# Kernel tuning notes

Measured on AMD Instinct MI355X. Metric: run time of the kernel, lower is better.

Reference implementation:

```python
import jax, jax.numpy as jnp
import numpy as np

B, T, D, U = 2, 512, 768, 768


def setup_inputs() -> dict:
    key = jax.random.key(0)
    kx, kv, ku, kw = jax.random.split(key, 4)
    x = jax.random.normal(kx, (B, T, D), dtype=jnp.float32)
    # glorot-ish scaled params
    V_a = jax.random.normal(kv, (U,), dtype=jnp.float32) * (1.0 / np.sqrt(U))
    U_a = jax.random.normal(ku, (D, U), dtype=jnp.float32) * (1.0 / np.sqrt(D))
    b_u = jnp.zeros((U,), dtype=jnp.float32)
    W_a = jax.random.normal(kw, (D, U), dtype=jnp.float32) * (1.0 / np.sqrt(D))
    return {"x": x, "V_a": V_a, "U_a": U_a, "b_u": b_u, "W_a": W_a}


def reference(x, V_a, U_a, b_u, W_a):
    # Bahdanau additive self-attention, fully batched (replaces the per-timestep loop).
    # wx[b,i,u] = x[b,i] @ W_a  (query projection; original recomputed this per step)
    wx = jnp.einsum('bid,du->biu', x, W_a)
    # ux[b,j,u] = x[b,j] @ U_a + b_u  (the _uxpb term)
    ux = jnp.einsum('bjd,du->bju', x, U_a) + b_u
    # e[b,i,j] = V_a . tanh(wx[b,i] + ux[b,j])
    e = jnp.einsum('biju,u->bij', jnp.tanh(wx[:, :, None, :] + ux[:, None, :, :]), V_a)
    # original: exp / sum over keys == softmax over axis j (no mask path)
    at = jax.nn.softmax(e, axis=2)
    # context[b,i,d] = sum_j at[b,i,j] * x[b,j,d]
    return jnp.einsum('bij,bjd->bid', at, x)
```

## Files before the change

kernel.cpp:

```cpp
#include <hip/hip_runtime.h>
#include <hip/hip_bf16.h>

#define BB 2
#define TT 512
#define DD 768
#define UU 768
#define NR (BB*TT)
#define CC 2.8853900817779268f

typedef __attribute__((ext_vector_type(8))) short short8v;
typedef __attribute__((ext_vector_type(4))) float float4v;
typedef __attribute__((ext_vector_type(4))) unsigned short ushort4v;

static __device__ __forceinline__ float fexp2(float x) { return __builtin_amdgcn_exp2f(x); }
static __device__ __forceinline__ float frcp(float x)  { return __builtin_amdgcn_rcpf(x); }
static __device__ __forceinline__ float readlane_f(float v, int l) {
    return __builtin_bit_cast(float, __builtin_amdgcn_readlane(__builtin_bit_cast(unsigned, v), l));
}
static __device__ __forceinline__ unsigned short bf16rn(float f) {
    unsigned u = __builtin_bit_cast(unsigned, f);
    u += 0x7FFFu + ((u >> 16) & 1u);
    return (unsigned short)(u >> 16);
}
static __device__ __forceinline__ float bf16tof(unsigned short h) {
    return __builtin_bit_cast(float, ((unsigned)h) << 16);
}

__global__ __launch_bounds__(256) void prep_split(
    const float* __restrict__ x,
    const float* __restrict__ Wm,
    const float* __restrict__ Um,
    unsigned short* __restrict__ xhi, unsigned short* __restrict__ xlo,
    unsigned short* __restrict__ WThi, unsigned short* __restrict__ WTlo,
    unsigned short* __restrict__ UThi, unsigned short* __restrict__ UTlo)
{
    const int mode = blockIdx.z;
    const int t = threadIdx.x;

    if (mode == 2) {
        const int blk = blockIdx.y * 12 + blockIdx.x;
        const float4* src = (const float4*)x + (size_t)blk * 1024;
        #pragma unroll
        for (int i = 0; i < 4; ++i) {
            const int idx = i * 256 + t;
            const float4 v = src[idx];
            ushort4v h, l;
            h.x = bf16rn(v.x); l.x = bf16rn(v.x - bf16tof(h.x));
            h.y = bf16rn(v.y); l.y = bf16rn(v.y - bf16tof(h.y));
            h.z = bf16rn(v.z); l.z = bf16rn(v.z - bf16tof(h.z));
            h.w = bf16rn(v.w); l.w = bf16rn(v.w - bf16tof(h.w));
            const size_t off = (size_t)blk * 4096 + (size_t)idx * 4;
            *(ushort4v*)(xhi + off) = h;
            *(ushort4v*)(xlo + off) = l;
        }
        return;
    }
    if (blockIdx.y >= 12) return;

    const float* __restrict__ S = (mode == 0) ? Wm : Um;
    unsigned short* __restrict__ Thi = (mode == 0) ? WThi : UThi;
    unsigned short* __restrict__ Tlo = (mode == 0) ? WTlo : UTlo;

    __shared__ float tile[64][65];
    const int d0 = blockIdx.y * 64;
    const int u0 = blockIdx.x * 64;

    #pragma unroll
    for (int i = 0; i < 4; ++i) {
        const int f4 = i * 256 + t;
        const int r  = f4 >> 4;
        const int c4 = f4 & 15;
        const float4 v = *(const float4*)(S + (size_t)(d0 + r) * UU + u0 + c4 * 4);
        tile[r][c4 * 4 + 0] = v.x;
        tile[r][c4 * 4 + 1] = v.y;
        tile[r][c4 * 4 + 2] = v.z;
        tile[r][c4 * 4 + 3] = v.w;
    }
    __syncthreads();
    #pragma unroll
    for (int i = 0; i < 2; ++i) {
        const int cid = i * 256 + t;
        const int ur  = cid >> 3;
        const int kc  = cid & 7;
        short8v H, L;
        #pragma unroll
        for (int j = 0; j < 8; ++j) {
            const float f = tile[kc * 8 + j][ur];
            const unsigned short h = bf16rn(f);
            H[j] = (short)h;
            L[j] = (short)bf16rn(f - bf16tof(h));
        }
        const size_t off = (size_t)(u0 + ur) * DD + d0 + kc * 8;
        *(short8v*)(Thi + off) = H;
        *(short8v*)(Tlo + off) = L;
    }
}

__global__ __launch_bounds__(256) void gemm_mfma(
    const unsigned short* __restrict__ xhi, const unsigned short* __restrict__ xlo,
    const unsigned short* __restrict__ WThi, const unsigned short* __restrict__ WTlo,
    const unsigned short* __restrict__ UThi, const unsigned short* __restrict__ UTlo,
    const float* __restrict__ bu,
    float* __restrict__ EW4,
    float* __restrict__ EUT)
{
    const int mode = blockIdx.z;
    const unsigned short* __restrict__ Ahi = mode ? UThi : WThi;
    const unsigned short* __restrict__ Alo = mode ? UTlo : WTlo;

    __shared__ unsigned short lds[4 * 4096];

    const int tid  = threadIdx.x;
    const int lane = tid & 63;
    const int wid  = tid >> 6;
    const int wm   = wid >> 1, wn = wid & 1;
    const int u0   = blockIdx.y * 64;
    const int r0t  = blockIdx.x * 64;

    const int srow0 = tid >> 3;
    const int srow1 = srow0 + 32;
    const int sc0   = tid & 7;
    const int sw0   = (sc0 ^ (srow0 & 7)) << 3;

    short8v g0, g1, g2, g3, g4, g5, g6, g7;

#define LOADSTEP(K0) { \
    const size_t ka = (size_t)(K0) + sc0 * 8; \
    g0 = *(const short8v*)(Ahi + (size_t)(u0 + srow0) * DD + ka); \
    g1 = *(const short8v*)(Ahi + (size_t)(u0 + srow1) * DD + ka); \
    g2 = *(const short8v*)(Alo + (size_t)(u0 + srow0) * DD + ka); \
    g3 = *(const short8v*)(Alo + (size_t)(u0 + srow1) * DD + ka); \
    g4 = *(const short8v*)(xhi + (size_t)(r0t + srow0) * DD + ka); \
    g5 = *(const short8v*)(xhi + (size_t)(r0t + srow1) * DD + ka); \
    g6 = *(const short8v*)(xlo + (size_t)(r0t + srow0) * DD + ka); \
    g7 = *(const short8v*)(xlo + (size_t)(r0t + srow1) * DD + ka); }

#define WRITESTEP { \
    *(short8v*)&lds[0 * 4096 + srow0 * 64 + sw0] = g0; \
    *(short8v*)&lds[0 * 4096 + srow1 * 64 + sw0] = g1; \
    *(short8v*)&lds[1 * 4096 + srow0 * 64 + sw0] = g2; \
    *(short8v*)&lds[1 * 4096 + srow1 * 64 + sw0] = g3; \
    *(short8v*)&lds[2 * 4096 + srow0 * 64 + sw0] = g4; \
    *(short8v*)&lds[2 * 4096 + srow1 * 64 + sw0] = g5; \
    *(short8v*)&lds[3 * 4096 + srow0 * 64 + sw0] = g6; \
    *(short8v*)&lds[3 * 4096 + srow1 * 64 + sw0] = g7; }

    float4v acc[2][2] = {};

    LOADSTEP(0);
    for (int s = 0; s < 12; ++s) {
        __syncthreads();
        WRITESTEP;
        __syncthreads();
        if (s < 11) LOADSTEP((s + 1) * 64);

        short8v ah[2][2], al[2][2], bh[2][2], bl[2][2];
        #pragma unroll
        for (int f = 0; f < 2; ++f) {
            const int arow = wm * 32 + f * 16 + (lane & 15);
            const int brow = wn * 32 + f * 16 + (lane & 15);
            #pragma unroll
            for (int kk = 0; kk < 2; ++kk) {
                const int ck = kk * 4 + (lane >> 4);
                ah[f][kk] = *(const short8v*)&lds[0 * 4096 + arow * 64 + (((ck ^ (arow & 7))) << 3)];
                al[f][kk] = *(const short8v*)&lds[1 * 4096 + arow * 64 + (((ck ^ (arow & 7))) << 3)];
                bh[f][kk] = *(const short8v*)&lds[2 * 4096 + brow * 64 + (((ck ^ (brow & 7))) << 3)];
                bl[f][kk] = *(const short8v*)&lds[3 * 4096 + brow * 64 + (((ck ^ (brow & 7))) << 3)];
            }
        }
        #pragma unroll
        for (int kk = 0; kk < 2; ++kk)
            #pragma unroll
            for (int m = 0; m < 2; ++m)
                #pragma unroll
                for (int n = 0; n < 2; ++n) {
                    acc[m][n] = __builtin_amdgcn_mfma_f32_16x16x32_bf16(ah[m][kk], bh[n][kk], acc[m][n], 0, 0, 0);
                    acc[m][n] = __builtin_amdgcn_mfma_f32_16x16x32_bf16(ah[m][kk], bl[n][kk], acc[m][n], 0, 0, 0);
                    acc[m][n] = __builtin_amdgcn_mfma_f32_16x16x32_bf16(al[m][kk], bh[n][kk], acc[m][n], 0, 0, 0);
                }
    }

    #pragma unroll
    for (int m = 0; m < 2; ++m) {
        #pragma unroll
        for (int n = 0; n < 2; ++n) {
            const int ub = u0 + wm * 32 + m * 16 + ((lane >> 4) << 2);
            const int r  = r0t + wn * 32 + n * 16 + (lane & 15);
            if (mode == 0) {
                float* dst = EW4 + ((size_t)(r >> 2) * UU + ub) * 4 + (r & 3);
                #pragma unroll
                for (int reg = 0; reg < 4; ++reg)
                    dst[reg * 4] = fexp2(acc[m][n][reg] * CC);
            } else {
                const int b = r >> 9, j = r & 511;
                const float4 bv = *(const float4*)(bu + ub);
                float4v o;
                o[0] = fexp2((acc[m][n][0] + bv.x) * CC);
                o[1] = fexp2((acc[m][n][1] + bv.y) * CC);
                o[2] = fexp2((acc[m][n][2] + bv.z) * CC);
                o[3] = fexp2((acc[m][n][3] + bv.w) * CC);
                *(float4v*)(EUT + (size_t)b * (UU * TT) + (size_t)(ub >> 2) * (TT * 4) + j * 4) = o;
            }
        }
    }
#undef LOADSTEP
#undef WRITESTEP
}

__global__ __launch_bounds__(512) void attn_fused(
    const float* __restrict__ x,
    const float* __restrict__ V_a,
    const float* __restrict__ EW4,
    const float* __restrict__ EUT,
    float* __restrict__ out)
{
    extern __shared__ float smem[];
    float* part = smem;
    float* red  = smem;

    const int tid  = threadIdx.x;
    const int lane = tid & 63;
    const int w    = tid >> 6;

    const int bid = blockIdx.x;
    const int blk = (bid & 7) * 32 + (bid >> 3);

    const int r0 = blk * 4;
    const int b  = r0 >> 9;

    const float4* __restrict__ ew4q = (const float4*)EW4 + (size_t)blk * UU;
    const float4* __restrict__ vp4  = (const float4*)V_a;
    const float4* __restrict__ eq   = (const float4*)(EUT + (size_t)b * UU * TT) + tid;

    float acc0 = 0.f, acc1 = 0.f, acc2 = 0.f, acc3 = 0.f;

#define ROW4(E4, S0, S1, S2, S3, V4, F, ACC) { \
    const float d0 = fmaf((E4).x, S0.F, 1.f); \
    const float d1 = fmaf((E4).y, S1.F, 1.f); \
    const float d2 = fmaf((E4).z, S2.F, 1.f); \
    const float d3 = fmaf((E4).w, S3.F, 1.f); \
    float n01 = (V4).x * d1; n01 = fmaf((V4).y, d0, n01); \
    float n23 = (V4).z * d3; n23 = fmaf((V4).w, d2, n23); \
    const float dd01 = d0 * d1, dd23 = d2 * d3; \
    float n = n01 * dd23; n = fmaf(n23, dd01, n); \
    ACC = fmaf(n, frcp(dd01 * dd23), ACC); }
#define QUAD4(E4, q) { \
    const float4 S0 = ew4q[4 * (q)]; \
    const float4 S1 = ew4q[4 * (q) + 1]; \
    const float4 S2 = ew4q[4 * (q) + 2]; \
    const float4 S3 = ew4q[4 * (q) + 3]; \
    const float4 V4 = vp4[(q)]; \
    ROW4(E4, S0, S1, S2, S3, V4, x, acc0); \
    ROW4(E4, S0, S1, S2, S3, V4, y, acc1); \
    ROW4(E4, S0, S1, S2, S3, V4, z, acc2); \
    ROW4(E4, S0, S1, S2, S3, V4, w, acc3); }

    float4 c0 = eq[0 * 512], c1 = eq[1 * 512], c2 = eq[2 * 512], c3 = eq[3 * 512];
    #pragma unroll 1
    for (int c = 0; c < 47; ++c) {
        const int q = 4 * c;
        float4 n0_ = eq[(size_t)(q + 4) * 512];
        float4 n1_ = eq[(size_t)(q + 5) * 512];
        float4 n2_ = eq[(size_t)(q + 6) * 512];
        float4 n3_ = eq[(size_t)(q + 7) * 512];
        QUAD4(c0, q); QUAD4(c1, q + 1); QUAD4(c2, q + 2); QUAD4(c3, q + 3);
        c0 = n0_; c1 = n1_; c2 = n2_; c3 = n3_;
    }
    QUAD4(c0, 188); QUAD4(c1, 189); QUAD4(c2, 190); QUAD4(c3, 191);
#undef QUAD4
#undef ROW4

    float m0 = acc0, m1 = acc1, m2 = acc2, m3 = acc3;
    #pragma unroll
    for (int off = 32; off; off >>= 1) {
        m0 = fminf(m0, __shfl_xor(m0, off, 64));
        m1 = fminf(m1, __shfl_xor(m1, off, 64));
        m2 = fminf(m2, __shfl_xor(m2, off, 64));
        m3 = fminf(m3, __shfl_xor(m3, off, 64));
    }
    if (lane == 0) {
        red[0 * 8 + w] = m0; red[1 * 8 + w] = m1;
        red[2 * 8 + w] = m2; red[3 * 8 + w] = m3;
    }
    __syncthreads();
    float M0 = red[0], M1 = red[8], M2 = red[16], M3 = red[24];
    #pragma unroll
    for (int k = 1; k < 8; ++k) {
        M0 = fminf(M0, red[0 * 8 + k]);
        M1 = fminf(M1, red[1 * 8 + k]);
        M2 = fminf(M2, red[2 * 8 + k]);
        M3 = fminf(M3, red[3 * 8 + k]);
    }

    const float p0 = fexp2(CC * (M0 - acc0));
    const float p1 = fexp2(CC * (M1 - acc1));
    const float p2 = fexp2(CC * (M2 - acc2));
    const float p3 = fexp2(CC * (M3 - acc3));
    float s0 = p0, s1 = p1, s2 = p2, s3 = p3;
    #pragma unroll
    for (int off = 32; off; off >>= 1) {
        s0 += __shfl_xor(s0, off, 64);
        s1 += __shfl_xor(s1, off, 64);
        s2 += __shfl_xor(s2, off, 64);
        s3 += __shfl_xor(s3, off, 64);
    }
    __syncthreads();
    if (lane == 0) {
        red[32 + 0 * 8 + w] = s0; red[32 + 1 * 8 + w] = s1;
        red[32 + 2 * 8 + w] = s2; red[32 + 3 * 8 + w] = s3;
    }
    __syncthreads();
    float S0 = red[32], S1 = red[40], S2 = red[48], S3 = red[56];
    #pragma unroll
    for (int k = 1; k < 8; ++k) {
        S0 += red[32 + k];
        S1 += red[40 + k];
        S2 += red[48 + k];
        S3 += red[56 + k];
    }
    const float i0 = frcp(S0), i1 = frcp(S1), i2 = frcp(S2), i3 = frcp(S3);

    const float* __restrict__ xb = x + (size_t)b * TT * DD + (size_t)w * 64 * DD + 4 * lane;
    float4 z4 = {0.f, 0.f, 0.f, 0.f};
    float4 pc00 = z4, pc01 = z4, pc02 = z4;
    float4 pc10 = z4, pc11 = z4, pc12 = z4;
    float4 pc20 = z4, pc21 = z4, pc22 = z4;
    float4 pc30 = z4, pc31 = z4, pc32 = z4;

#define F4(dst, a, xv) { dst.x = fmaf(a, xv.x, dst.x); dst.y = fmaf(a, xv.y, dst.y); \
                         dst.z = fmaf(a, xv.z, dst.z); dst.w = fmaf(a, xv.w, dst.w); }
    #pragma unroll 2
    for (int jj = 0; jj < 64; ++jj) {
        const float a0 = readlane_f(p0, jj);
        const float a1 = readlane_f(p1, jj);
        const float a2 = readlane_f(p2, jj);
        const float a3 = readlane_f(p3, jj);
        const float* xr = xb + (size_t)jj * DD;
        const float4 x0 = *(const float4*)(xr);
        const float4 x1 = *(const float4*)(xr + 256);
        const float4 x2 = *(const float4*)(xr + 512);
        F4(pc00, a0, x0); F4(pc01, a0, x1); F4(pc02, a0, x2);
        F4(pc10, a1, x0); F4(pc11, a1, x1); F4(pc12, a1, x2);
        F4(pc20, a2, x0); F4(pc21, a2, x1); F4(pc22, a2, x2);
        F4(pc30, a3, x0); F4(pc31, a3, x1); F4(pc32, a3, x2);
    }
#undef F4

    __syncthreads();
    {
        float* pw = part + w * 1536 + 4 * lane;
        *(float4*)(pw + 0)    = pc00;
        *(float4*)(pw + 256)  = pc01;
        *(float4*)(pw + 512)  = pc02;
        *(float4*)(pw + 768)  = pc10;
        *(float4*)(pw + 1024) = pc11;
        *(float4*)(pw + 1280) = pc12;
    }
    __syncthreads();
    #pragma unroll
    for (int e = 0; e < 3; ++e) {
        const int idx = e * 512 + tid;
        const int r   = (idx >= 768) ? 1 : 0;
        const int d   = idx - r * 768;
        float ssum = 0.f;
        #pragma unroll
        for (int w2 = 0; w2 < 8; ++w2) ssum += part[w2 * 1536 + r * 768 + d];
        out[(size_t)(r0 + r) * DD + d] = ssum * (r ? i1 : i0);
    }
    __syncthreads();
    {
        float* pw = part + w * 1536 + 4 * lane;
        *(float4*)(pw + 0)    = pc20;
        *(float4*)(pw + 256)  = pc21;
        *(float4*)(pw + 512)  = pc22;
        *(float4*)(pw + 768)  = pc30;
        *(float4*)(pw + 1024) = pc31;
        *(float4*)(pw + 1280) = pc32;
    }
    __syncthreads();
    #pragma unroll
    for (int e = 0; e < 3; ++e) {
        const int idx = e * 512 + tid;
        const int r   = (idx >= 768) ? 1 : 0;
        const int d   = idx - r * 768;
        float ssum = 0.f;
        #pragma unroll
        for (int w2 = 0; w2 < 8; ++w2) ssum += part[w2 * 1536 + r * 768 + d];
        out[(size_t)(r0 + 2 + r) * DD + d] = ssum * (r ? i3 : i2);
    }
}

extern "C" void kernel_launch(void* const* d_in, const int* in_sizes, int n_in,
                              void* d_out, int out_size, void* d_ws, size_t ws_size,
                              hipStream_t stream)
{
    const float* x   = (const float*)d_in[0];
    const float* V_a = (const float*)d_in[1];
    const float* U_a = (const float*)d_in[2];
    const float* b_u = (const float*)d_in[3];
    const float* W_a = (const float*)d_in[4];
    float* out = (float*)d_out;

    float* EW4 = (float*)d_ws;
    float* EUT = EW4 + (size_t)UU * NR;
    unsigned short* xhi  = (unsigned short*)(EUT + (size_t)BB * UU * TT);
    unsigned short* xlo  = xhi + (size_t)NR * DD;
    unsigned short* WThi = xlo + (size_t)NR * DD;
    unsigned short* WTlo = WThi + (size_t)UU * DD;
    unsigned short* UThi = WTlo + (size_t)UU * DD;
    unsigned short* UTlo = UThi + (size_t)UU * DD;

    hipLaunchKernelGGL(prep_split, dim3(12, 16, 3), dim3(256), 0, stream,
                       x, W_a, U_a, xhi, xlo, WThi, WTlo, UThi, UTlo);

    hipLaunchKernelGGL(gemm_mfma, dim3(16, 12, 2), dim3(256), 0, stream,
                       xhi, xlo, WThi, WTlo, UThi, UTlo, b_u, EW4, EUT);

    const int ldsB = 12288 * sizeof(float);
    hipLaunchKernelGGL(attn_fused, dim3(NR / 4), dim3(512), ldsB, stream,
                       x, V_a, EW4, EUT, out);
}
```

Before: 76.72 us.

## Move attention-weighted context product to split-bf16 MFMA GEMM kernel

The fused attention kernel no longer computes the context product with scalar FMAs over x. It now writes the normalized attention weights as hi/lo bf16 pairs to a workspace. A new pv_mfma kernel then computes context = at·x with bf16 MFMA using a three-term split to keep near-fp32 accuracy. The prep kernel gains a mode that produces transposed hi/lo bf16 copies of x. The aim is to replace the FMA-bound context loop with matrix-core throughput, at the cost of an extra kernel launch and round-tripping the attention weights through global memory.

Measured after the change: 79.70 us. +3.9%, slower.

```diff
diff --git a/kernel.cpp b/kernel.cpp
--- a/kernel.cpp
+++ b/kernel.cpp
@@ -14,9 +14,6 @@
 
 static __device__ __forceinline__ float fexp2(float x) { return __builtin_amdgcn_exp2f(x); }
 static __device__ __forceinline__ float frcp(float x)  { return __builtin_amdgcn_rcpf(x); }
-static __device__ __forceinline__ float readlane_f(float v, int l) {
-    return __builtin_bit_cast(float, __builtin_amdgcn_readlane(__builtin_bit_cast(unsigned, v), l));
-}
 static __device__ __forceinline__ unsigned short bf16rn(float f) {
     unsigned u = __builtin_bit_cast(unsigned, f);
     u += 0x7FFFu + ((u >> 16) & 1u);
@@ -32,7 +29,8 @@
     const float* __restrict__ Um,
     unsigned short* __restrict__ xhi, unsigned short* __restrict__ xlo,
     unsigned short* __restrict__ WThi, unsigned short* __restrict__ WTlo,
-    unsigned short* __restrict__ UThi, unsigned short* __restrict__ UTlo)
+    unsigned short* __restrict__ UThi, unsigned short* __restrict__ UTlo,
+    unsigned short* __restrict__ xThi, unsigned short* __restrict__ xTlo)
 {
     const int mode = blockIdx.z;
     const int t = threadIdx.x;
@@ -55,6 +53,43 @@
         }
         return;
     }
+
+    if (mode == 3) {
+        __shared__ float tile[64][65];
+        const int j0 = blockIdx.y * 64;
+        const int d0 = blockIdx.x * 64;
+        #pragma unroll
+        for (int i = 0; i < 4; ++i) {
+            const int f4 = i * 256 + t;
+            const int r  = f4 >> 4;
+            const int c4 = f4 & 15;
+            const float4 v = *(const float4*)(x + (size_t)(j0 + r) * DD + d0 + c4 * 4);
+            tile[r][c4 * 4 + 0] = v.x;
+            tile[r][c4 * 4 + 1] = v.y;
+            tile[r][c4 * 4 + 2] = v.z;
+            tile[r][c4 * 4 + 3] = v.w;
+        }
+        __syncthreads();
+        #pragma unroll
+        for (int i = 0; i < 2; ++i) {
+            const int cid = i * 256 + t;
+            const int ur  = cid >> 3;
+            const int kc  = cid & 7;
+            short8v H, L;
+            #pragma unroll
+            for (int jj = 0; jj < 8; ++jj) {
+                const float f = tile[kc * 8 + jj][ur];
+                const unsigned short h = bf16rn(f);
+                H[jj] = (short)h;
+                L[jj] = (short)bf16rn(f - bf16tof(h));
+            }
+            const size_t off = (size_t)(d0 + ur) * NR + j0 + kc * 8;
+            *(short8v*)(xThi + off) = H;
+            *(short8v*)(xTlo + off) = L;
+        }
+        return;
+    }
+
     if (blockIdx.y >= 12) return;
 
     const float* __restrict__ S = (mode == 0) ? Wm : Um;
@@ -84,11 +119,11 @@
         const int kc  = cid & 7;
         short8v H, L;
         #pragma unroll
-        for (int j = 0; j < 8; ++j) {
-            const float f = tile[kc * 8 + j][ur];
+        for (int jj = 0; jj < 8; ++jj) {
+            const float f = tile[kc * 8 + jj][ur];
             const unsigned short h = bf16rn(f);
-            H[j] = (short)h;
-            L[j] = (short)bf16rn(f - bf16tof(h));
+            H[jj] = (short)h;
+            L[jj] = (short)bf16rn(f - bf16tof(h));
         }
         const size_t off = (size_t)(u0 + ur) * DD + d0 + kc * 8;
         *(short8v*)(Thi + off) = H;
@@ -207,16 +242,14 @@
 #undef WRITESTEP
 }
 
-__global__ __launch_bounds__(512) void attn_fused(
-    const float* __restrict__ x,
+__global__ __launch_bounds__(512) void attn_esm(
     const float* __restrict__ V_a,
     const float* __restrict__ EW4,
     const float* __restrict__ EUT,
-    float* __restrict__ out)
+    unsigned short* __restrict__ athi,
+    unsigned short* __restrict__ atlo)
 {
-    extern __shared__ float smem[];
-    float* part = smem;
-    float* red  = smem;
+    __shared__ float red[64];
 
     const int tid  = threadIdx.x;
     const int lane = tid & 63;
@@ -320,74 +353,107 @@
     }
     const float i0 = frcp(S0), i1 = frcp(S1), i2 = frcp(S2), i3 = frcp(S3);
 
-    const float* __restrict__ xb = x + (size_t)b * TT * DD + (size_t)w * 64 * DD + 4 * lane;
-    float4 z4 = {0.f, 0.f, 0.f, 0.f};
-    float4 pc00 = z4, pc01 = z4, pc02 = z4;
-    float4 pc10 = z4, pc11 = z4, pc12 = z4;
-    float4 pc20 = z4, pc21 = z4, pc22 = z4;
-    float4 pc30 = z4, pc31 = z4, pc32 = z4;
-
-#define F4(dst, a, xv) { dst.x = fmaf(a, xv.x, dst.x); dst.y = fmaf(a, xv.y, dst.y); \
-                         dst.z = fmaf(a, xv.z, dst.z); dst.w = fmaf(a, xv.w, dst.w); }
-    #pragma unroll 2
-    for (int jj = 0; jj < 64; ++jj) {
-        const float a0 = readlane_f(p0, jj);
-        const float a1 = readlane_f(p1, jj);
-        const float a2 = readlane_f(p2, jj);
-        const float a3 = readlane_f(p3, jj);
-        const float* xr = xb + (size_t)jj * DD;
-        const float4 x0 = *(const float4*)(xr);
-        const float4 x1 = *(const float4*)(xr + 256);
-        const float4 x2 = *(const float4*)(xr + 512);
-        F4(pc00, a0, x0); F4(pc01, a0, x1); F4(pc02, a0, x2);
-        F4(pc10, a1, x0); F4(pc11, a1, x1); F4(pc12, a1, x2);
-        F4(pc20, a2, x0); F4(pc21, a2, x1); F4(pc22, a2, x2);
-        F4(pc30, a3, x0); F4(pc31, a3, x1); F4(pc32, a3, x2);
-    }
-#undef F4
-
-    __syncthreads();
-    {
-        float* pw = part + w * 1536 + 4 * lane;
-        *(float4*)(pw + 0)    = pc00;
-        *(float4*)(pw + 256)  = pc01;
-        *(float4*)(pw + 512)  = pc02;
-        *(float4*)(pw + 768)  = pc10;
-        *(float4*)(pw + 1024) = pc11;
-        *(float4*)(pw + 1280) = pc12;
-    }
-    __syncthreads();
-    #pragma unroll
-    for (int e = 0; e < 3; ++e) {
-        const int idx = e * 512 + tid;
-        const int r   = (idx >= 768) ? 1 : 0;
-        const int d   = idx - r * 768;
-        float ssum = 0.f;
-        #pragma unroll
-        for (int w2 = 0; w2 < 8; ++w2) ssum += part[w2 * 1536 + r * 768 + d];
-        out[(size_t)(r0 + r) * DD + d] = ssum * (r ? i1 : i0);
-    }
-    __syncthreads();
-    {
-        float* pw = part + w * 1536 + 4 * lane;
-        *(float4*)(pw + 0)    = pc20;
-        *(float4*)(pw + 256)  = pc21;
-        *(float4*)(pw + 512)  = pc22;
-        *(float4*)(pw + 768)  = pc30;
-        *(float4*)(pw + 1024) = pc31;
-        *(float4*)(pw + 1280) = pc32;
-    }
-    __syncthreads();
-    #pragma unroll
-    for (int e = 0; e < 3; ++e) {
-        const int idx = e * 512 + tid;
-        const int r   = (idx >= 768) ? 1 : 0;
-        const int d   = idx - r * 768;
-        float ssum = 0.f;
-        #pragma unroll
-        for (int w2 = 0; w2 < 8; ++w2) ssum += part[w2 * 1536 + r * 768 + d];
-        out[(size_t)(r0 + 2 + r) * DD + d] = ssum * (r ? i3 : i2);
-    }
+    const float a0 = p0 * i0, a1 = p1 * i1, a2 = p2 * i2, a3 = p3 * i3;
+#define STORE_AT(R, A) { \
+    const unsigned short h = bf16rn(A); \
+    athi[(size_t)(r0 + (R)) * TT + tid] = h; \
+    atlo[(size_t)(r0 + (R)) * TT + tid] = bf16rn((A) - bf16tof(h)); }
+    STORE_AT(0, a0); STORE_AT(1, a1); STORE_AT(2, a2); STORE_AT(3, a3);
+#undef STORE_AT
+}
+
+__global__ __launch_bounds__(256) void pv_mfma(
+    const unsigned short* __restrict__ xThi, const unsigned short* __restrict__ xTlo,
+    const unsigned short* __restrict__ athi, const unsigned short* __restrict__ atlo,
+    float* __restrict__ out)
+{
+    __shared__ unsigned short lds[4 * 4096];
+
+    const int tid  = threadIdx.x;
+    const int lane = tid & 63;
+    const int wid  = tid >> 6;
+    const int wm   = wid >> 1, wn = wid & 1;
+    const int d0t  = blockIdx.y * 64;
+    const int i0t  = blockIdx.x * 64;
+    const int b    = i0t >> 9;
+
+    const int srow0 = tid >> 3;
+    const int srow1 = srow0 + 32;
+    const int sc0   = tid & 7;
+    const int sw0   = (sc0 ^ (srow0 & 7)) << 3;
+
+    short8v g0, g1, g2, g3, g4, g5, g6, g7;
+
+#define LOADSTEP(K0) { \
+    const size_t ka = (size_t)(K0) + sc0 * 8; \
+    g0 = *(const short8v*)(xThi + (size_t)(d0t + srow0) * NR + b * TT + ka); \
+    g1 = *(const short8v*)(xThi + (size_t)(d0t + srow1) * NR + b * TT + ka); \
+    g2 = *(const short8v*)(xTlo + (size_t)(d0t + srow0) * NR + b * TT + ka); \
+    g3 = *(const short8v*)(xTlo + (size_t)(d0t + srow1) * NR + b * TT + ka); \
+    g4 = *(const short8v*)(athi + (size_t)(i0t + srow0) * TT + ka); \
+    g5 = *(const short8v*)(athi + (size_t)(i0t + srow1) * TT + ka); \
+    g6 = *(const short8v*)(atlo + (size_t)(i0t + srow0) * TT + ka); \
+    g7 = *(const short8v*)(atlo + (size_t)(i0t + srow1) * TT + ka); }
+
+#define WRITESTEP { \
+    *(short8v*)&lds[0 * 4096 + srow0 * 64 + sw0] = g0; \
+    *(short8v*)&lds[0 * 4096 + srow1 * 64 + sw0] = g1; \
+    *(short8v*)&lds[1 * 4096 + srow0 * 64 + sw0] = g2; \
+    *(short8v*)&lds[1 * 4096 + srow1 * 64 + sw0] = g3; \
+    *(short8v*)&lds[2 * 4096 + srow0 * 64 + sw0] = g4; \
+    *(short8v*)&lds[2 * 4096 + srow1 * 64 + sw0] = g5; \
+    *(short8v*)&lds[3 * 4096 + srow0 * 64 + sw0] = g6; \
+    *(short8v*)&lds[3 * 4096 + srow1 * 64 + sw0] = g7; }
+
+    float4v acc[2][2] = {};
+
+    LOADSTEP(0);
+    for (int s = 0; s < 8; ++s) {
+        __syncthreads();
+        WRITESTEP;
+        __syncthreads();
+        if (s < 7) LOADSTEP((s + 1) * 64);
+
+        short8v ah[2][2], al[2][2], bh[2][2], bl[2][2];
+        #pragma unroll
+        for (int f = 0; f < 2; ++f) {
+            const int arow = wm * 32 + f * 16 + (lane & 15);
+            const int brow = wn * 32 + f * 16 + (lane & 15);
+            #pragma unroll
+            for (int kk = 0; kk < 2; ++kk) {
+                const int ck = kk * 4 + (lane >> 4);
+                ah[f][kk] = *(const short8v*)&lds[0 * 4096 + arow * 64 + (((ck ^ (arow & 7))) << 3)];
+                al[f][kk] = *(const short8v*)&lds[1 * 4096 + arow * 64 + (((ck ^ (arow & 7))) << 3)];
+                bh[f][kk] = *(const short8v*)&lds[2 * 4096 + brow * 64 + (((ck ^ (brow & 7))) << 3)];
+                bl[f][kk] = *(const short8v*)&lds[3 * 4096 + brow * 64 + (((ck ^ (brow & 7))) << 3)];
+            }
+        }
+        #pragma unroll
+        for (int kk = 0; kk < 2; ++kk)
+            #pragma unroll
+            for (int m = 0; m < 2; ++m)
+                #pragma unroll
+                for (int n = 0; n < 2; ++n) {
+                    acc[m][n] = __builtin_amdgcn_mfma_f32_16x16x32_bf16(ah[m][kk], bh[n][kk], acc[m][n], 0, 0, 0);
+                    acc[m][n] = __builtin_amdgcn_mfma_f32_16x16x32_bf16(ah[m][kk], bl[n][kk], acc[m][n], 0, 0, 0);
+                    acc[m][n] = __builtin_amdgcn_mfma_f32_16x16x32_bf16(al[m][kk], bh[n][kk], acc[m][n], 0, 0, 0);
+                }
+    }
+
+    #pragma unroll
+    for (int m = 0; m < 2; ++m) {
+        #pragma unroll
+        for (int n = 0; n < 2; ++n) {
+            const int db = d0t + wm * 32 + m * 16 + ((lane >> 4) << 2);
+            const int i  = i0t + wn * 32 + n * 16 + (lane & 15);
+            float4v o;
+            o[0] = acc[m][n][0]; o[1] = acc[m][n][1];
+            o[2] = acc[m][n][2]; o[3] = acc[m][n][3];
+            *(float4v*)(out + (size_t)i * DD + db) = o;
+        }
+    }
+#undef LOADSTEP
+#undef WRITESTEP
 }
 
 extern "C" void kernel_launch(void* const* d_in, const int* in_sizes, int n_in,
@@ -409,14 +475,20 @@
     unsigned short* WTlo = WThi + (size_t)UU * DD;
     unsigned short* UThi = WTlo + (size_t)UU * DD;
     unsigned short* UTlo = UThi + (size_t)UU * DD;
-
-    hipLaunchKernelGGL(prep_split, dim3(12, 16, 3), dim3(256), 0, stream,
-                       x, W_a, U_a, xhi, xlo, WThi, WTlo, UThi, UTlo);
+    unsigned short* xThi = UTlo + (size_t)UU * DD;
+    unsigned short* xTlo = xThi + (size_t)DD * NR;
+    unsigned short* athi = xTlo + (size_t)DD * NR;
+    unsigned short* atlo = athi + (size_t)NR * TT;
+
+    hipLaunchKernelGGL(prep_split, dim3(12, 16, 4), dim3(256), 0, stream,
+                       x, W_a, U_a, xhi, xlo, WThi, WTlo, UThi, UTlo, xThi, xTlo);
 
     hipLaunchKernelGGL(gemm_mfma, dim3(16, 12, 2), dim3(256), 0, stream,
                        xhi, xlo, WThi, WTlo, UThi, UTlo, b_u, EW4, EUT);
 
-    const int ldsB = 12288 * sizeof(float);
-    hipLaunchKernelGGL(attn_fused, dim3(NR / 4), dim3(512), ldsB, stream,
-                       x, V_a, EW4, EUT, out);
-}
+    hipLaunchKernelGGL(attn_esm, dim3(NR / 4), dim3(512), 0, stream,
+                       V_a, EW4, EUT, athi, atlo);
+
+    hipLaunchKernelGGL(pv_mfma, dim3(16, 12), dim3(256), 0, stream,
+                       xThi, xTlo, athi, atlo, out);
+}
```
